# Kernel tuning notes

Hardware: AMD Instinct MI355X
Metric: run time of the kernel (lower is better)

Reference implementation:

```python
import jax, jax.numpy as jnp
import numpy as np

N_ITERS = 30  # sinkhorn iterations, matching torch default


def sinkhorn(log_alpha, n_iters=N_ITERS):
    # log_alpha: (B, N, K) -> approximately doubly-stochastic (B, N, K)
    x = log_alpha - jnp.max(log_alpha, axis=(-2, -1), keepdims=True)
    x = jnp.exp(x)
    for _ in range(n_iters):
        x = x / (jnp.sum(x, axis=-1, keepdims=True) + 1e-8)  # row normalize
        x = x / (jnp.sum(x, axis=-2, keepdims=True) + 1e-8)  # col normalize
    return x


def greedy_unique_argmax(scores):
    # scores: (B, N, K) with N == K. Returns hard permutation matrix (B, N, K).
    B, N, K = scores.shape

    def one(s):  # s: (N, K)
        order = jnp.argsort(-s.reshape(-1))  # flat indices, descending score

        def body(carry, idx):
            used_r, used_c, assign = carry
            r = idx // K
            c = idx % K
            take = jnp.logical_not(used_r[r] | used_c[c])
            used_r = used_r.at[r].set(used_r[r] | take)
            used_c = used_c.at[c].set(used_c[c] | take)
            assign = assign.at[r].set(jnp.where(take, c, assign[r]))
            return (used_r, used_c, assign), None

        init = (jnp.zeros((N,), jnp.bool_),
                jnp.zeros((K,), jnp.bool_),
                jnp.full((N,), 0, jnp.int32))
        (_, _, assign), _ = jax.lax.scan(body, init, order)
        return jax.nn.one_hot(assign, K, dtype=s.dtype)

    return jax.vmap(one)(scores)


def setup_inputs() -> dict:
    key = jax.random.key(0)
    B, N, K = 4096, 64, 64
    cell_logits = jax.random.normal(key, (B, N, K), dtype=jnp.float32)
    pos_temp = jnp.asarray(1.1, dtype=jnp.float32)  # softplus(pos_temp_raw)+1e-6 at init
    return {"cell_logits": cell_logits, "pos_temp": pos_temp}


def reference(cell_logits, pos_temp):
    logits = cell_logits / (pos_temp + 1e-6)
    w_soft = sinkhorn(logits, N_ITERS)
    w_hard = greedy_unique_argmax(jax.lax.stop_gradient(w_soft))
    # straight-through: forward = hard permutation, backward = soft sinkhorn grads
    w = w_hard + (w_soft - jax.lax.stop_gradient(w_soft))
    return w
```

## Files before the change

kernel.cpp:

```cpp
#include <hip/hip_runtime.h>
#include <cstdint>
#include <cstddef>


typedef float f2 __attribute__((ext_vector_type(2)));

__device__ __forceinline__ f2 fma2(f2 a, f2 b, f2 c) {
#if defined(__has_builtin) && __has_builtin(__builtin_elementwise_fma)
    return __builtin_elementwise_fma(a, b, c);
#else
    f2 r; r.x = __builtin_fmaf(a.x, b.x, c.x); r.y = __builtin_fmaf(a.y, b.y, c.y);
    return r;
#endif
}

#define RESCAN(G)                                                            \
  {                                                                          \
    float nv_ = -__builtin_inff(); int na_ = (G) * 8;                        \
    _Pragma("unroll")                                                        \
    for (int k_ = 0; k_ < 8; ++k_) {                                         \
      const int idx_ = (G) * 8 + k_;                                         \
      float vk_ = ((rowmask >> idx_) & 1ull) ? col[idx_]                     \
                                             : -__builtin_inff();            \
      if (vk_ > nv_) { nv_ = vk_; na_ = idx_; }                              \
    }                                                                        \
    gv[(G)] = nv_; ga[(G)] = na_;                                            \
  }

#define RESCAN_SWITCH(RG)                                                    \
    switch (RG) {                                                            \
        case 0: RESCAN(0) break;                                             \
        case 1: RESCAN(1) break;                                             \
        case 2: RESCAN(2) break;                                             \
        case 3: RESCAN(3) break;                                             \
        case 4: RESCAN(4) break;                                             \
        case 5: RESCAN(5) break;                                             \
        case 6: RESCAN(6) break;                                             \
        case 7: RESCAN(7) break;                                             \
    }

__global__ void __launch_bounds__(64)
__attribute__((amdgpu_waves_per_eu(1)))
sinkhorn_perm_kernel(const float* __restrict__ logits,
                     const float* __restrict__ ptemp,
                     float* __restrict__ out)
{
    __shared__ __attribute__((aligned(16))) float bufU[64];
    __shared__ __attribute__((aligned(16))) float bufV[64];

    const int b    = blockIdx.x;
    const int lane = threadIdx.x;
    const float* base = logits + (size_t)b * 4096;

    const float T    = ptemp[0] + 1e-6f;
    const float invT = 1.0f / T;

    f2 row2[32];
    {
        const float4* rp = (const float4*)(base + lane * 64);
        #pragma unroll
        for (int t = 0; t < 16; ++t) {
            float4 q = rp[t];
            row2[2*t+0].x = __fmul_rn(q.x, invT);
            row2[2*t+0].y = __fmul_rn(q.y, invT);
            row2[2*t+1].x = __fmul_rn(q.z, invT);
            row2[2*t+1].y = __fmul_rn(q.w, invT);
        }
    }

    float mx = row2[0].x;
    #pragma unroll
    for (int i = 0; i < 32; ++i) { mx = fmaxf(mx, row2[i].x); mx = fmaxf(mx, row2[i].y); }
    #pragma unroll
    for (int w = 1; w <= 32; w <<= 1)
        mx = fmaxf(mx, __shfl_xor(mx, w, 64));

    #pragma unroll
    for (int i = 0; i < 32; ++i) {
        row2[i].x = __expf(__fsub_rn(row2[i].x, mx));
        row2[i].y = __expf(__fsub_rn(row2[i].y, mx));
    }

    float col[64];
    #pragma unroll
    for (int i = 0; i < 64; ++i) {
        float raw = base[i * 64 + lane];
        col[i] = __expf(__fsub_rn(__fmul_rn(raw, invT), mx));
    }

    const float4* bu4 = (const float4*)bufU;
    const float4* bv4 = (const float4*)bufV;

    float u = 1.0f, v = 1.0f;
    for (int it = 0; it < 30; ++it) {
        bufV[lane] = v;
        f2 A0 = {0.f, 0.f}, A1 = {0.f, 0.f};
        #pragma unroll
        for (int t = 0; t < 16; ++t) {
            float4 q = bv4[t];
            f2 qa = { q.x, q.y };
            f2 qb = { q.z, q.w };
            A0 = fma2(row2[2*t+0], qa, A0);
            A1 = fma2(row2[2*t+1], qb, A1);
        }
        float rs = __fadd_rn(__fadd_rn(A0.x, A0.y), __fadd_rn(A1.x, A1.y));
        u = u / __fadd_rn(__fmul_rn(u, rs), 1e-8f);

        bufU[lane] = u;
        A0 = (f2){0.f, 0.f}; A1 = (f2){0.f, 0.f};
        #pragma unroll
        for (int t = 0; t < 16; ++t) {
            float4 q = bu4[t];
            f2 ca = { col[4*t+0], col[4*t+1] };
            f2 cb = { col[4*t+2], col[4*t+3] };
            f2 qa = { q.x, q.y };
            f2 qb = { q.z, q.w };
            A0 = fma2(ca, qa, A0);
            A1 = fma2(cb, qb, A1);
        }
        float cs = __fadd_rn(__fadd_rn(A0.x, A0.y), __fadd_rn(A1.x, A1.y));
        v = v / __fadd_rn(__fmul_rn(v, cs), 1e-8f);
    }

    #pragma unroll
    for (int t = 0; t < 16; ++t) {
        float4 q = bu4[t];
        col[4*t+0] = __fmul_rn(__fmul_rn(col[4*t+0], q.x), v);
        col[4*t+1] = __fmul_rn(__fmul_rn(col[4*t+1], q.y), v);
        col[4*t+2] = __fmul_rn(__fmul_rn(col[4*t+2], q.z), v);
        col[4*t+3] = __fmul_rn(__fmul_rn(col[4*t+3], q.w), v);
    }

    unsigned long long rowmask = ~0ull;
    float gv[8]; int ga[8];
    #pragma unroll
    for (int g = 0; g < 8; ++g) RESCAN(g)

    int  mycol   = 0;
    bool done    = false;
    int  retired = 0;
    const float NEGINF = -__builtin_inff();

    while (retired < 64) {
        float bv = gv[0]; int ba = ga[0];
        #pragma unroll
        for (int g2 = 1; g2 < 8; ++g2)
            if (gv[g2] > bv) { bv = gv[g2]; ba = ga[g2]; }
        float mybv = done ? NEGINF : bv;

        float m1 = mybv, m2 = NEGINF;
        #pragma unroll
        for (int m = 1; m <= 32; m <<= 1) {
            float o1 = __shfl_xor(m1, m, 64);
            float o2 = __shfl_xor(m2, m, 64);
            float hi = fmaxf(m1, o1);
            float lo = fminf(m1, o1);
            m1 = hi;
            m2 = fmaxf(lo, fmaxf(m2, o2));
        }

        int r1, c1, r2 = -1, c2 = -1;
        bool two = false;
        unsigned long long t1 = __ballot(mybv == m1);
        bool fast1 = (__popcll(t1) == 1) && (m2 > NEGINF);

        if (fast1) {
            c1 = (int)__builtin_ctzll(t1);
            r1 = __builtin_amdgcn_readlane(ba, c1);
            unsigned long long t2 = __ballot(mybv == m2);
            if (__popcll(t2) == 1) {
                c2 = (int)__builtin_ctzll(t2);
                r2 = __builtin_amdgcn_readlane(ba, c2);
                two = (r2 != r1);
            }
        } else {
            unsigned flat = ((unsigned)ba << 6) | (unsigned)lane;
            unsigned long long key =
                ((unsigned long long)__float_as_uint(bv) << 12) | (4095u - flat);
            if (done) key = 0ull;
            #pragma unroll
            for (int m = 1; m <= 32; m <<= 1) {
                unsigned long long o = __shfl_xor(key, m, 64);
                if (o > key) key = o;
            }
            unsigned wflat = 4095u - (unsigned)(key & 4095ull);
            r1 = __builtin_amdgcn_readfirstlane((int)(wflat >> 6));
            c1 = (int)(wflat & 63u);
        }

        if (lane == r1) mycol = c1;
        if (lane == c1) done  = true;
        rowmask &= ~(1ull << r1);
        retired++;
        if (two) {
            if (lane == r2) mycol = c2;
            if (lane == c2) done  = true;
            rowmask &= ~(1ull << r2);
            retired++;
        }

        RESCAN_SWITCH(r1 >> 3)
        if (two && ((r2 >> 3) != (r1 >> 3))) {
            RESCAN_SWITCH(r2 >> 3)
        }
    }

    float* orow = out + (size_t)b * 4096 + lane * 64;
    #pragma unroll
    for (int t = 0; t < 16; ++t) {
        float4 q;
        q.x = (4*t+0 == mycol) ? 1.0f : 0.0f;
        q.y = (4*t+1 == mycol) ? 1.0f : 0.0f;
        q.z = (4*t+2 == mycol) ? 1.0f : 0.0f;
        q.w = (4*t+3 == mycol) ? 1.0f : 0.0f;
        ((float4*)orow)[t] = q;
    }
}

extern "C" void kernel_launch(void* const* d_in, const int* in_sizes, int n_in,
                              void* d_out, int out_size, void* d_ws, size_t ws_size,
                              hipStream_t stream) {
    const float* logits = (const float*)d_in[0];
    const float* ptemp  = (const float*)d_in[1];
    float* out = (float*)d_out;
    const int B = in_sizes[0] / 4096;
    sinkhorn_perm_kernel<<<B, 64, 0, stream>>>(logits, ptemp, out);
}
```

Measured before the change: 214.0 us.

## Replace greedy global-max selection with mutual-best-pair matching rounds

The sequential greedy assignment, which found the global maximum through wave-wide shuffles one or two entries at a time, is replaced by a parallel scheme. Each round, every active row finds its best free column and every active column finds its best free row. Pairs that pick each other are committed together, since a mutual best is a greedy pick. This cuts the number of serial rounds at the cost of full 64-wide scans per round and an extra row rescale. The tie-breaking and the positive-value masking trick (0 as the floor) may differ from the reference when values tie or are zero, and the round cap of 64 is assumed to be enough.

```diff
diff --git a/kernel.cpp b/kernel.cpp
--- a/kernel.cpp
+++ b/kernel.cpp
@@ -13,31 +13,6 @@
     return r;
 #endif
 }
-
-#define RESCAN(G)                                                            \
-  {                                                                          \
-    float nv_ = -__builtin_inff(); int na_ = (G) * 8;                        \
-    _Pragma("unroll")                                                        \
-    for (int k_ = 0; k_ < 8; ++k_) {                                         \
-      const int idx_ = (G) * 8 + k_;                                         \
-      float vk_ = ((rowmask >> idx_) & 1ull) ? col[idx_]                     \
-                                             : -__builtin_inff();            \
-      if (vk_ > nv_) { nv_ = vk_; na_ = idx_; }                              \
-    }                                                                        \
-    gv[(G)] = nv_; ga[(G)] = na_;                                            \
-  }
-
-#define RESCAN_SWITCH(RG)                                                    \
-    switch (RG) {                                                            \
-        case 0: RESCAN(0) break;                                             \
-        case 1: RESCAN(1) break;                                             \
-        case 2: RESCAN(2) break;                                             \
-        case 3: RESCAN(3) break;                                             \
-        case 4: RESCAN(4) break;                                             \
-        case 5: RESCAN(5) break;                                             \
-        case 6: RESCAN(6) break;                                             \
-        case 7: RESCAN(7) break;                                             \
-    }
 
 __global__ void __launch_bounds__(64)
 __attribute__((amdgpu_waves_per_eu(1)))
@@ -130,79 +105,50 @@
         col[4*t+2] = __fmul_rn(__fmul_rn(col[4*t+2], q.z), v);
         col[4*t+3] = __fmul_rn(__fmul_rn(col[4*t+3], q.w), v);
     }
+    bufV[lane] = v;
+    #pragma unroll
+    for (int t = 0; t < 16; ++t) {
+        float4 q = bv4[t];
+        row2[2*t+0].x = __fmul_rn(__fmul_rn(row2[2*t+0].x, u), q.x);
+        row2[2*t+0].y = __fmul_rn(__fmul_rn(row2[2*t+0].y, u), q.y);
+        row2[2*t+1].x = __fmul_rn(__fmul_rn(row2[2*t+1].x, u), q.z);
+        row2[2*t+1].y = __fmul_rn(__fmul_rn(row2[2*t+1].y, u), q.w);
+    }
 
     unsigned long long rowmask = ~0ull;
-    float gv[8]; int ga[8];
-    #pragma unroll
-    for (int g = 0; g < 8; ++g) RESCAN(g)
+    unsigned long long colmask = ~0ull;
+    int mycol  = 0;
+    int rounds = 0;
 
-    int  mycol   = 0;
-    bool done    = false;
-    int  retired = 0;
-    const float NEGINF = -__builtin_inff();
+    while (rowmask && rounds < 64) {
+        ++rounds;
 
-    while (retired < 64) {
-        float bv = gv[0]; int ba = ga[0];
+        float rbv = 0.0f; int rbj = 0;
         #pragma unroll
-        for (int g2 = 1; g2 < 8; ++g2)
-            if (gv[g2] > bv) { bv = gv[g2]; ba = ga[g2]; }
-        float mybv = done ? NEGINF : bv;
-
-        float m1 = mybv, m2 = NEGINF;
-        #pragma unroll
-        for (int m = 1; m <= 32; m <<= 1) {
-            float o1 = __shfl_xor(m1, m, 64);
-            float o2 = __shfl_xor(m2, m, 64);
-            float hi = fmaxf(m1, o1);
-            float lo = fminf(m1, o1);
-            m1 = hi;
-            m2 = fmaxf(lo, fmaxf(m2, o2));
+        for (int j = 0; j < 64; ++j) {
+            unsigned sm = ((colmask >> j) & 1ull) ? 0xFFFFFFFFu : 0u;
+            float sv = (j & 1) ? row2[j >> 1].y : row2[j >> 1].x;
+            float s  = __uint_as_float(__float_as_uint(sv) & sm);
+            if (s > rbv) { rbv = s; rbj = j; }
         }
 
-        int r1, c1, r2 = -1, c2 = -1;
-        bool two = false;
-        unsigned long long t1 = __ballot(mybv == m1);
-        bool fast1 = (__popcll(t1) == 1) && (m2 > NEGINF);
-
-        if (fast1) {
-            c1 = (int)__builtin_ctzll(t1);
-            r1 = __builtin_amdgcn_readlane(ba, c1);
-            unsigned long long t2 = __ballot(mybv == m2);
-            if (__popcll(t2) == 1) {
-                c2 = (int)__builtin_ctzll(t2);
-                r2 = __builtin_amdgcn_readlane(ba, c2);
-                two = (r2 != r1);
-            }
-        } else {
-            unsigned flat = ((unsigned)ba << 6) | (unsigned)lane;
-            unsigned long long key =
-                ((unsigned long long)__float_as_uint(bv) << 12) | (4095u - flat);
-            if (done) key = 0ull;
-            #pragma unroll
-            for (int m = 1; m <= 32; m <<= 1) {
-                unsigned long long o = __shfl_xor(key, m, 64);
-                if (o > key) key = o;
-            }
-            unsigned wflat = 4095u - (unsigned)(key & 4095ull);
-            r1 = __builtin_amdgcn_readfirstlane((int)(wflat >> 6));
-            c1 = (int)(wflat & 63u);
+        float cbv = 0.0f; int cbi = 0;
+        #pragma unroll
+        for (int i = 0; i < 64; ++i) {
+            unsigned sm = ((rowmask >> i) & 1ull) ? 0xFFFFFFFFu : 0u;
+            float s  = __uint_as_float(__float_as_uint(col[i]) & sm);
+            if (s > cbv) { cbv = s; cbi = i; }
         }
 
-        if (lane == r1) mycol = c1;
-        if (lane == c1) done  = true;
-        rowmask &= ~(1ull << r1);
-        retired++;
-        if (two) {
-            if (lane == r2) mycol = c2;
-            if (lane == c2) done  = true;
-            rowmask &= ~(1ull << r2);
-            retired++;
-        }
-
-        RESCAN_SWITCH(r1 >> 3)
-        if (two && ((r2 >> 3) != (r1 >> 3))) {
-            RESCAN_SWITCH(r2 >> 3)
-        }
+        int gr = __builtin_amdgcn_ds_bpermute(rbj << 2, cbi);
+        int gc = __builtin_amdgcn_ds_bpermute(cbi << 2, rbj);
+        bool aR = (rowmask >> lane) & 1ull;
+        bool aC = (colmask >> lane) & 1ull;
+        bool mr = aR && (gr == lane);
+        bool mc = aC && (gc == lane);
+        if (mr) mycol = rbj;
+        rowmask &= ~__ballot(mr);
+        colmask &= ~__ballot(mc);
     }
 
     float* orow = out + (size_t)b * 4096 + lane * 64;
```

Result: faster. 179.7 us (-16.0%).
